# Performance work log

Hardware: AMD Instinct MI355X
Metric: run time of the kernel (lower is better)

Reference implementation:

```python
import jax, jax.numpy as jnp
import numpy as np

HIDDEN = 2048
INTER = 5632
B, S = 2, 2048


def _ternary(key, shape):
    # values in {-1, 0, +1}, matching 2-bit packed ternary weights
    return jax.random.randint(key, shape, -1, 2).astype(jnp.float32)


def setup_inputs() -> dict:
    key = jax.random.key(0)
    ks = jax.random.split(key, 7)
    x = jax.random.normal(ks[0], (B, S, HIDDEN), dtype=jnp.float32)
    gate_w = _ternary(ks[1], (INTER, HIDDEN))   # [intermediate, hidden]
    up_w = _ternary(ks[2], (INTER, HIDDEN))     # [intermediate, hidden]
    down_w = _ternary(ks[3], (HIDDEN, INTER))   # [hidden, intermediate]
    # per-output-channel dequant scales (positive, as from absmean quantization)
    gate_s = jax.random.uniform(ks[4], (INTER,), minval=0.01, maxval=0.1, dtype=jnp.float32)
    up_s = jax.random.uniform(ks[5], (INTER,), minval=0.01, maxval=0.1, dtype=jnp.float32)
    down_s = jax.random.uniform(ks[6], (HIDDEN,), minval=0.01, maxval=0.1, dtype=jnp.float32)
    return {"x": x, "gate_w": gate_w, "up_w": up_w, "down_w": down_w,
            "gate_s": gate_s, "up_s": up_s, "down_s": down_s}


def reference(x, gate_w, up_w, down_w, gate_s, up_s, down_s):
    # x: (B, S, H) -> flatten tokens, as in forward_hidden
    b, s, h = x.shape
    xf = x.reshape(b * s, h)
    # ternary linear = add/sub-only matmul + per-channel scale
    g = jnp.einsum('th,ih->ti', xf, gate_w) * gate_s   # (T, I)
    u = jnp.einsum('th,ih->ti', xf, up_w) * up_s       # (T, I)
    hdn = jax.nn.silu(g) * u                            # gated activation
    out = jnp.einsum('ti,hi->th', hdn, down_w) * down_s  # (T, H)
    return out.reshape(b, s, -1)
```

## Files before the change

### kernel.cpp

```cpp
#include <hip/hip_runtime.h>
#include <stdint.h>
#include <stddef.h>

#define HIDDEN 2048
#define INTER  5632
#define TOKENS 4096
#define BKD    128
#define BKI    128

typedef __attribute__((ext_vector_type(8))) _Float16 f16x8;
typedef __attribute__((ext_vector_type(4))) _Float16 f16x4;
typedef __attribute__((ext_vector_type(4))) float    f32x4;
typedef __attribute__((ext_vector_type(4))) int      i32x4;

__device__ __forceinline__ int swz8(int row, int q) {
    return row * 8 + ((q + row) & 7);
}

#define GLDS16(g, l) __builtin_amdgcn_global_load_lds( \
    (__attribute__((address_space(1))) void*)(g), \
    (__attribute__((address_space(3))) void*)(l), 16, 0, 0)

__global__ __launch_bounds__(256)
void prepass(const float* __restrict__ x,
             const float4* __restrict__ gw, const float4* __restrict__ uw,
             const float4* __restrict__ dw,
             int8_t* __restrict__ xq, float* __restrict__ xs,
             int* __restrict__ go, int* __restrict__ uo,
             f16x4* __restrict__ dno) {
    const int tid = threadIdx.x;
    if (blockIdx.x < TOKENS) {
        const int t = blockIdx.x;
        const float4* row = (const float4*)(x + (size_t)t * HIDDEN);
        float4 v0 = row[tid * 2];
        float4 v1 = row[tid * 2 + 1];
        float m = fmaxf(fmaxf(fabsf(v0.x), fabsf(v0.y)), fmaxf(fabsf(v0.z), fabsf(v0.w)));
        m = fmaxf(m, fmaxf(fmaxf(fabsf(v1.x), fabsf(v1.y)), fmaxf(fabsf(v1.z), fabsf(v1.w))));
        #pragma unroll
        for (int off = 32; off; off >>= 1)
            m = fmaxf(m, __shfl_xor(m, off, 64));
        __shared__ float wmax[4];
        if ((tid & 63) == 0) wmax[tid >> 6] = m;
        __syncthreads();
        m = fmaxf(fmaxf(wmax[0], wmax[1]), fmaxf(wmax[2], wmax[3]));
        m = fmaxf(m, 1e-20f);
        if (tid == 0) xs[t] = m * (1.0f / 127.0f);
        const float inv = 127.0f / m;
        float vals[8] = {v0.x, v0.y, v0.z, v0.w, v1.x, v1.y, v1.z, v1.w};
        int b[8];
        #pragma unroll
        for (int i = 0; i < 8; ++i) b[i] = (int)rintf(vals[i] * inv);
        int lo = (b[0] & 255) | ((b[1] & 255) << 8) | ((b[2] & 255) << 16) | (b[3] << 24);
        int hi = (b[4] & 255) | ((b[5] & 255) << 8) | ((b[6] & 255) << 16) | (b[7] << 24);
        ((int2*)(xq + (size_t)t * HIDDEN))[tid] = make_int2(lo, hi);
        return;
    }
    const int NW4 = INTER * HIDDEN / 4;
    int i = (blockIdx.x - TOKENS) * blockDim.x + tid;
    const int stride = 2048 * blockDim.x;
    for (; i < 3 * NW4; i += stride) {
        if (i < 2 * NW4) {
            const bool is_g = i < NW4;
            const int j = is_g ? i : i - NW4;
            float4 f = is_g ? gw[j] : uw[j];
            int p = ((int)(signed char)(int)f.x & 255)
                  | (((int)(signed char)(int)f.y & 255) << 8)
                  | (((int)(signed char)(int)f.z & 255) << 16)
                  | (((int)(signed char)(int)f.w) << 24);
            if (is_g) go[j] = p; else uo[j] = p;
        } else {
            const int j = i - 2 * NW4;
            float4 f = dw[j];
            f16x4 o;
            o.x = (_Float16)f.x; o.y = (_Float16)f.y;
            o.z = (_Float16)f.z; o.w = (_Float16)f.w;
            dno[j] = o;
        }
    }
}

__global__ __launch_bounds__(512, 2)
void gemm_gateup(const int8_t* __restrict__ Xq,
                 const int8_t* __restrict__ Wg,
                 const int8_t* __restrict__ Wu,
                 const float* __restrict__ xs,
                 const float* __restrict__ gs,
                 const float* __restrict__ us,
                 _Float16* __restrict__ Hm) {
    __shared__ int8_t As [256 * BKI];
    __shared__ int8_t Bgs[128 * BKI];
    __shared__ int8_t Bus[128 * BKI];

    const int pid = (blockIdx.x % 8) * 88 + blockIdx.x / 8;
    const int bm  = (pid & 15) * 256;
    const int bn  = (pid >> 4) * 128;

    const int tid  = threadIdx.x;
    const int lane = tid & 63;
    const int wave = tid >> 6;
    const int wm   = (wave >> 1) * 64;
    const int wn   = (wave & 1) * 64;
    const int l15  = lane & 15;
    const int lq   = lane >> 4;

    int rowA[4], sgA[4];
    #pragma unroll
    for (int j = 0; j < 4; ++j) {
        const int f = tid + 512 * j;
        rowA[j] = f >> 3;
        sgA[j]  = (((f & 7) - rowA[j]) & 7) * 16;
    }

    const int8_t* gA = Xq + (size_t)bm * HIDDEN;
    const int8_t* gG = Wg + (size_t)bn * HIDDEN;
    const int8_t* gU = Wu + (size_t)bn * HIDDEN;

    i32x4 accg[4][4] = {};
    i32x4 accu[4][4] = {};

    for (int k0 = 0; k0 < HIDDEN; k0 += BKI) {
        #pragma unroll
        for (int j = 0; j < 4; ++j) {
            const int f = tid + 512 * j;
            GLDS16(gA + (size_t)rowA[j] * HIDDEN + k0 + sgA[j], &As[f * 16]);
        }
        #pragma unroll
        for (int j = 0; j < 2; ++j) {
            const int f = tid + 512 * j;
            const size_t off = (size_t)rowA[j] * HIDDEN + k0 + sgA[j];
            GLDS16(gG + off, &Bgs[f * 16]);
            GLDS16(gU + off, &Bus[f * 16]);
        }
        __syncthreads();

        #pragma unroll
        for (int ks = 0; ks < 2; ++ks) {
            const int q = ks * 4 + lq;
            i32x4 a[4];
            #pragma unroll
            for (int im = 0; im < 4; ++im)
                a[im] = *(const i32x4*)&As[swz8(wm + im * 16 + l15, q) * 16];
            #pragma unroll
            for (int jn = 0; jn < 4; ++jn) {
                i32x4 bg = *(const i32x4*)&Bgs[swz8(wn + jn * 16 + l15, q) * 16];
                i32x4 bu = *(const i32x4*)&Bus[swz8(wn + jn * 16 + l15, q) * 16];
                #pragma unroll
                for (int im = 0; im < 4; ++im) {
                    accg[im][jn] = __builtin_amdgcn_mfma_i32_16x16x64_i8(a[im], bg, accg[im][jn], 0, 0, 0);
                    accu[im][jn] = __builtin_amdgcn_mfma_i32_16x16x64_i8(a[im], bu, accu[im][jn], 0, 0, 0);
                }
            }
        }
        __syncthreads();
    }

    #pragma unroll
    for (int jn = 0; jn < 4; ++jn) {
        const int col = bn + wn + jn * 16 + l15;
        const float sg = gs[col];
        const float su = us[col];
        #pragma unroll
        for (int im = 0; im < 4; ++im) {
            const int rbase = bm + wm + im * 16 + lq * 4;
            #pragma unroll
            for (int r = 0; r < 4; ++r) {
                const int row = rbase + r;
                const float st = xs[row];
                float g = (float)accg[im][jn][r] * st * sg;
                float u = (float)accu[im][jn][r] * st * su;
                float h = (g / (1.0f + __expf(-g))) * u;
                Hm[(size_t)row * INTER + col] = (_Float16)h;
            }
        }
    }
}

__global__ __launch_bounds__(256, 2)
void gemm_down(const _Float16* __restrict__ Hm,
               const _Float16* __restrict__ Wd,
               const float* __restrict__ dsc,
               float* __restrict__ out) {
    __shared__ _Float16 As0[128 * 64];
    __shared__ _Float16 As1[128 * 64];
    __shared__ _Float16 Bs0[128 * 64];
    __shared__ _Float16 Bs1[128 * 64];

    const int pid = (blockIdx.x % 8) * 64 + blockIdx.x / 8;
    const int loc = pid & 255;
    const int bm  = ((pid >> 8) * 16 + (loc & 15)) * 128;
    const int bn  = (loc >> 4) * 128;

    const int tid  = threadIdx.x;
    const int lane = tid & 63;
    const int wave = tid >> 6;
    const int wm   = (wave >> 1) * 64;
    const int wn   = (wave & 1) * 64;
    const int l15  = lane & 15;
    const int lq   = lane >> 4;

    int rS[4], sS[4];
    #pragma unroll
    for (int j = 0; j < 4; ++j) {
        const int f = tid + 256 * j;
        rS[j] = f >> 3;
        sS[j] = (((f & 7) - (f >> 3)) & 7) * 8;
    }

    const _Float16* gA = Hm + (size_t)bm * INTER;
    const _Float16* gB = Wd + (size_t)bn * INTER;

    f32x4 acc[4][4] = {};

    for (int k0 = 0; k0 < INTER; k0 += BKD) {
        #pragma unroll
        for (int j = 0; j < 4; ++j) {
            const int f = tid + 256 * j;
            const size_t oA = (size_t)rS[j] * INTER + k0 + sS[j];
            GLDS16(gA + oA,      &As0[f * 8]);
            GLDS16(gA + oA + 64, &As1[f * 8]);
            const size_t oB = (size_t)rS[j] * INTER + k0 + sS[j];
            GLDS16(gB + oB,      &Bs0[f * 8]);
            GLDS16(gB + oB + 64, &Bs1[f * 8]);
        }
        __syncthreads();

        #pragma unroll
        for (int ks = 0; ks < 4; ++ks) {
            const _Float16* A_ = (ks < 2) ? As0 : As1;
            const _Float16* B_ = (ks < 2) ? Bs0 : Bs1;
            const int q = (ks & 1) * 4 + lq;
            f16x8 a[4];
            #pragma unroll
            for (int im = 0; im < 4; ++im)
                a[im] = *(const f16x8*)&A_[swz8(wm + im * 16 + l15, q) * 8];
            #pragma unroll
            for (int jn = 0; jn < 4; ++jn) {
                f16x8 b = *(const f16x8*)&B_[swz8(wn + jn * 16 + l15, q) * 8];
                #pragma unroll
                for (int im = 0; im < 4; ++im)
                    acc[im][jn] = __builtin_amdgcn_mfma_f32_16x16x32_f16(a[im], b, acc[im][jn], 0, 0, 0);
            }
        }
        __syncthreads();
    }

    #pragma unroll
    for (int jn = 0; jn < 4; ++jn) {
        const int col = bn + wn + jn * 16 + l15;
        const float sd = dsc[col];
        #pragma unroll
        for (int im = 0; im < 4; ++im) {
            const int rbase = bm + wm + im * 16 + lq * 4;
            #pragma unroll
            for (int r = 0; r < 4; ++r)
                out[(size_t)(rbase + r) * HIDDEN + col] = acc[im][jn][r] * sd;
        }
    }
}

extern "C" void kernel_launch(void* const* d_in, const int* in_sizes, int n_in,
                              void* d_out, int out_size, void* d_ws, size_t ws_size,
                              hipStream_t stream) {
    const float* x   = (const float*)d_in[0];
    const float* gw  = (const float*)d_in[1];
    const float* uw  = (const float*)d_in[2];
    const float* dw  = (const float*)d_in[3];
    const float* gsc = (const float*)d_in[4];
    const float* usc = (const float*)d_in[5];
    const float* dsc = (const float*)d_in[6];
    float* out = (float*)d_out;

    char* ws = (char*)d_ws;
    int8_t*   Xq  = (int8_t*)(ws);
    int8_t*   Wg8 = (int8_t*)(ws + 8388608ull);
    int8_t*   Wu8 = (int8_t*)(ws + 19922944ull);
    _Float16* Wdh = (_Float16*)(ws + 31457280ull);
    _Float16* Hm  = (_Float16*)(ws + 54525952ull);
    float*    xs  = (float*)(ws + 100663296ull);

    prepass<<<TOKENS + 2048, 256, 0, stream>>>(
        x, (const float4*)gw, (const float4*)uw, (const float4*)dw,
        Xq, xs, (int*)Wg8, (int*)Wu8, (f16x4*)Wdh);

    gemm_gateup<<<(INTER / 128) * (TOKENS / 256), 512, 0, stream>>>(
        Xq, Wg8, Wu8, xs, gsc, usc, Hm);
    gemm_down<<<(HIDDEN / 128) * (TOKENS / 128), 256, 0, stream>>>(
        Hm, Wdh, dsc, out);
}
```

Before: 387.2 us.

## Shrink gate/up GEMM tile to 128x128 and vectorize prepass conversions

The gate/up GEMM moves from 256-token tiles with 512 threads to 128x128 tiles with 256 threads. This doubles the grid, and a new block swizzle groups blocks by token chunk. The prepass now quantizes one token per wave with no shared-memory reduction or block barrier, and weight conversion writes 16-byte vectors per thread instead of 4- or 8-byte ones. The smaller tile lowers LDS use and raises occupancy, but each block reuses the weight tiles over fewer tokens, so more global traffic goes to reloading them.

```diff
diff --git a/kernel.cpp b/kernel.cpp
--- a/kernel.cpp
+++ b/kernel.cpp
@@ -20,6 +20,13 @@
 #define GLDS16(g, l) __builtin_amdgcn_global_load_lds( \
     (__attribute__((address_space(1))) void*)(g), \
     (__attribute__((address_space(3))) void*)(l), 16, 0, 0)
+
+__device__ __forceinline__ int pack4i8(float4 f) {
+    return ((int)(signed char)(int)f.x & 255)
+         | (((int)(signed char)(int)f.y & 255) << 8)
+         | (((int)(signed char)(int)f.z & 255) << 16)
+         | (((int)(signed char)(int)f.w) << 24);
+}
 
 __global__ __launch_bounds__(256)
 void prepass(const float* __restrict__ x,
@@ -27,59 +34,67 @@
              const float4* __restrict__ dw,
              int8_t* __restrict__ xq, float* __restrict__ xs,
              int* __restrict__ go, int* __restrict__ uo,
-             f16x4* __restrict__ dno) {
+             _Float16* __restrict__ dno) {
     const int tid = threadIdx.x;
-    if (blockIdx.x < TOKENS) {
-        const int t = blockIdx.x;
+    if (blockIdx.x < 1024) {
+        const int wave = tid >> 6;
+        const int lane = tid & 63;
+        const int t    = blockIdx.x * 4 + wave;
         const float4* row = (const float4*)(x + (size_t)t * HIDDEN);
-        float4 v0 = row[tid * 2];
-        float4 v1 = row[tid * 2 + 1];
-        float m = fmaxf(fmaxf(fabsf(v0.x), fabsf(v0.y)), fmaxf(fabsf(v0.z), fabsf(v0.w)));
-        m = fmaxf(m, fmaxf(fmaxf(fabsf(v1.x), fabsf(v1.y)), fmaxf(fabsf(v1.z), fabsf(v1.w))));
+        float4 v[8];
+        #pragma unroll
+        for (int j = 0; j < 8; ++j) v[j] = row[lane + 64 * j];
+        float m = 0.0f;
+        #pragma unroll
+        for (int j = 0; j < 8; ++j) {
+            m = fmaxf(m, fmaxf(fmaxf(fabsf(v[j].x), fabsf(v[j].y)),
+                               fmaxf(fabsf(v[j].z), fabsf(v[j].w))));
+        }
         #pragma unroll
         for (int off = 32; off; off >>= 1)
             m = fmaxf(m, __shfl_xor(m, off, 64));
-        __shared__ float wmax[4];
-        if ((tid & 63) == 0) wmax[tid >> 6] = m;
-        __syncthreads();
-        m = fmaxf(fmaxf(wmax[0], wmax[1]), fmaxf(wmax[2], wmax[3]));
         m = fmaxf(m, 1e-20f);
-        if (tid == 0) xs[t] = m * (1.0f / 127.0f);
+        if (lane == 0) xs[t] = m * (1.0f / 127.0f);
         const float inv = 127.0f / m;
-        float vals[8] = {v0.x, v0.y, v0.z, v0.w, v1.x, v1.y, v1.z, v1.w};
-        int b[8];
-        #pragma unroll
-        for (int i = 0; i < 8; ++i) b[i] = (int)rintf(vals[i] * inv);
-        int lo = (b[0] & 255) | ((b[1] & 255) << 8) | ((b[2] & 255) << 16) | (b[3] << 24);
-        int hi = (b[4] & 255) | ((b[5] & 255) << 8) | ((b[6] & 255) << 16) | (b[7] << 24);
-        ((int2*)(xq + (size_t)t * HIDDEN))[tid] = make_int2(lo, hi);
+        int* oq = (int*)(xq + (size_t)t * HIDDEN);
+        #pragma unroll
+        for (int j = 0; j < 8; ++j) {
+            float4 f = v[j];
+            f.x *= inv; f.y *= inv; f.z *= inv; f.w *= inv;
+            float4 r;
+            r.x = rintf(f.x); r.y = rintf(f.y); r.z = rintf(f.z); r.w = rintf(f.w);
+            oq[lane + 64 * j] = pack4i8(r);
+        }
         return;
     }
-    const int NW4 = INTER * HIDDEN / 4;
-    int i = (blockIdx.x - TOKENS) * blockDim.x + tid;
-    const int stride = 2048 * blockDim.x;
-    for (; i < 3 * NW4; i += stride) {
-        if (i < 2 * NW4) {
-            const bool is_g = i < NW4;
-            const int j = is_g ? i : i - NW4;
-            float4 f = is_g ? gw[j] : uw[j];
-            int p = ((int)(signed char)(int)f.x & 255)
-                  | (((int)(signed char)(int)f.y & 255) << 8)
-                  | (((int)(signed char)(int)f.z & 255) << 16)
-                  | (((int)(signed char)(int)f.w) << 24);
-            if (is_g) go[j] = p; else uo[j] = p;
+    const int NA = INTER * HIDDEN / 16;
+    const int NC = INTER * HIDDEN / 8;
+    const int stride = 2048 * 256;
+    for (int u = (blockIdx.x - 1024) * 256 + tid; u < 2 * NA + NC; u += stride) {
+        if (u < 2 * NA) {
+            const bool is_g = u < NA;
+            const int j = is_g ? u : u - NA;
+            const float4* src = (is_g ? gw : uw) + (size_t)j * 4;
+            float4 f0 = src[0], f1 = src[1], f2 = src[2], f3 = src[3];
+            int4 p;
+            p.x = pack4i8(f0); p.y = pack4i8(f1);
+            p.z = pack4i8(f2); p.w = pack4i8(f3);
+            ((int4*)(is_g ? go : uo))[j] = p;
         } else {
-            const int j = i - 2 * NW4;
-            float4 f = dw[j];
-            f16x4 o;
-            o.x = (_Float16)f.x; o.y = (_Float16)f.y;
-            o.z = (_Float16)f.z; o.w = (_Float16)f.w;
-            dno[j] = o;
-        }
-    }
-}
-
-__global__ __launch_bounds__(512, 2)
+            const int j = u - 2 * NA;
+            const float4* src = dw + (size_t)j * 2;
+            float4 a = src[0], b = src[1];
+            f16x8 o;
+            o[0] = (_Float16)a.x; o[1] = (_Float16)a.y;
+            o[2] = (_Float16)a.z; o[3] = (_Float16)a.w;
+            o[4] = (_Float16)b.x; o[5] = (_Float16)b.y;
+            o[6] = (_Float16)b.z; o[7] = (_Float16)b.w;
+            *(f16x8*)(dno + (size_t)j * 8) = o;
+        }
+    }
+}
+
+__global__ __launch_bounds__(256, 2)
 void gemm_gateup(const int8_t* __restrict__ Xq,
                  const int8_t* __restrict__ Wg,
                  const int8_t* __restrict__ Wu,
@@ -87,13 +102,14 @@
                  const float* __restrict__ gs,
                  const float* __restrict__ us,
                  _Float16* __restrict__ Hm) {
-    __shared__ int8_t As [256 * BKI];
+    __shared__ int8_t As [128 * BKI];
     __shared__ int8_t Bgs[128 * BKI];
     __shared__ int8_t Bus[128 * BKI];
 
-    const int pid = (blockIdx.x % 8) * 88 + blockIdx.x / 8;
-    const int bm  = (pid & 15) * 256;
-    const int bn  = (pid >> 4) * 128;
+    const int pid   = (blockIdx.x % 8) * 176 + blockIdx.x / 8;
+    const int local = pid % (16 * 44);
+    const int bm    = ((pid / (16 * 44)) * 16 + (local & 15)) * 128;
+    const int bn    = (local >> 4) * 128;
 
     const int tid  = threadIdx.x;
     const int lane = tid & 63;
@@ -106,30 +122,24 @@
     int rowA[4], sgA[4];
     #pragma unroll
     for (int j = 0; j < 4; ++j) {
-        const int f = tid + 512 * j;
+        const int f = tid + 256 * j;
         rowA[j] = f >> 3;
         sgA[j]  = (((f & 7) - rowA[j]) & 7) * 16;
     }
 
-    const int8_t* gA = Xq + (size_t)bm * HIDDEN;
-    const int8_t* gG = Wg + (size_t)bn * HIDDEN;
-    const int8_t* gU = Wu + (size_t)bn * HIDDEN;
-
     i32x4 accg[4][4] = {};
     i32x4 accu[4][4] = {};
 
     for (int k0 = 0; k0 < HIDDEN; k0 += BKI) {
         #pragma unroll
         for (int j = 0; j < 4; ++j) {
-            const int f = tid + 512 * j;
-            GLDS16(gA + (size_t)rowA[j] * HIDDEN + k0 + sgA[j], &As[f * 16]);
-        }
-        #pragma unroll
-        for (int j = 0; j < 2; ++j) {
-            const int f = tid + 512 * j;
-            const size_t off = (size_t)rowA[j] * HIDDEN + k0 + sgA[j];
-            GLDS16(gG + off, &Bgs[f * 16]);
-            GLDS16(gU + off, &Bus[f * 16]);
+            const int f = tid + 256 * j;
+            const int8_t* pX = Xq + (size_t)(bm + rowA[j]) * HIDDEN + k0 + sgA[j];
+            const int8_t* pG = Wg + (size_t)(bn + rowA[j]) * HIDDEN + k0 + sgA[j];
+            const int8_t* pU = Wu + (size_t)(bn + rowA[j]) * HIDDEN + k0 + sgA[j];
+            GLDS16(pX, &As [f * 16]);
+            GLDS16(pG, &Bgs[f * 16]);
+            GLDS16(pU, &Bus[f * 16]);
         }
         __syncthreads();
 
@@ -218,9 +228,8 @@
             const size_t oA = (size_t)rS[j] * INTER + k0 + sS[j];
             GLDS16(gA + oA,      &As0[f * 8]);
             GLDS16(gA + oA + 64, &As1[f * 8]);
-            const size_t oB = (size_t)rS[j] * INTER + k0 + sS[j];
-            GLDS16(gB + oB,      &Bs0[f * 8]);
-            GLDS16(gB + oB + 64, &Bs1[f * 8]);
+            GLDS16(gB + oA,      &Bs0[f * 8]);
+            GLDS16(gB + oA + 64, &Bs1[f * 8]);
         }
         __syncthreads();
 
@@ -278,11 +287,11 @@
     _Float16* Hm  = (_Float16*)(ws + 54525952ull);
     float*    xs  = (float*)(ws + 100663296ull);
 
-    prepass<<<TOKENS + 2048, 256, 0, stream>>>(
+    prepass<<<1024 + 2048, 256, 0, stream>>>(
         x, (const float4*)gw, (const float4*)uw, (const float4*)dw,
-        Xq, xs, (int*)Wg8, (int*)Wu8, (f16x4*)Wdh);
-
-    gemm_gateup<<<(INTER / 128) * (TOKENS / 256), 512, 0, stream>>>(
+        Xq, xs, (int*)Wg8, (int*)Wu8, Wdh);
+
+    gemm_gateup<<<(INTER / 128) * (TOKENS / 128), 256, 0, stream>>>(
         Xq, Wg8, Wu8, xs, gsc, usc, Hm);
     gemm_down<<<(HIDDEN / 128) * (TOKENS / 128), 256, 0, stream>>>(
         Hm, Wdh, dsc, out);
```

Result: faster. 371.2 us (-4.1%).
